# Optimization experiments

Measured on AMD Instinct MI355X. Metric: run time of the kernel, lower is better.

Reference implementation:

```python
import jax, jax.numpy as jnp
import numpy as np

N, B, T, S, E, R = 4, 8, 512, 512, 1024, 1024


def setup_inputs() -> dict:
    key = jax.random.key(0)
    k1, k2, k3, k4, k5 = jax.random.split(key, 5)
    return {
        "query": jax.random.normal(k1, (1, B, T, E), dtype=jnp.float32),
        "key_value_states": jax.random.normal(k2, (N, B, S, R), dtype=jnp.float32),
        "attention_mask": jax.random.normal(k3, (1, B, T, S), dtype=jnp.float32),
        "Wk": jax.random.normal(k4, (E, R), dtype=jnp.float32) * (1.0 / np.sqrt(R)),
        "bk": jax.random.normal(k5, (E,), dtype=jnp.float32) * 0.01,
    }


def reference(query, key_value_states, attention_mask, Wk, bk):
    # k_proj: [N,B,S,R] @ [R,E] + bias -> [N,B,S,E]
    key = jnp.einsum("nbsr,er->nbse", key_value_states, Wk) + bk
    # QK^T (no scaling), query broadcast over N: [N,B,T,S]
    scores = jnp.einsum("bte,nbse->nbts", query[0], key)
    scores = scores + attention_mask  # mask broadcast over N
    attn = jax.nn.softmax(scores, axis=-1)
    # weights @ raw key_value_states (NOT projected key): [N,B,T,R]
    out = jnp.einsum("nbts,nbsr->nbtr", attn, key_value_states)
    return out
```

## Files before the change

### kernel.cpp

```cpp
#include <hip/hip_runtime.h>

typedef unsigned short u16;
typedef unsigned int u32;
typedef unsigned long long u64;

typedef __bf16 bfrag __attribute__((ext_vector_type(8)));
typedef float f32x4 __attribute__((ext_vector_type(4)));

typedef __attribute__((address_space(1))) char* gas1_p;
typedef __attribute__((address_space(3))) char* las3_p;

#define DI __device__ __forceinline__

DI u16 f2bf(float f) {
  u32 u = __float_as_uint(f);
  u += 0x7FFFu + ((u >> 16) & 1u);
  return (u16)(u >> 16);
}
DI float bf2f(u16 h) { return __uint_as_float(((u32)h) << 16); }

DI void gload16(const void* g, void* l) {
  __builtin_amdgcn_global_load_lds((gas1_p)(u64)g, (las3_p)(u32)(u64)l, 16, 0, 0);
}

__global__ __launch_bounds__(256) void k_split4(const float4* __restrict__ in,
                                                uint2* __restrict__ hi,
                                                uint2* __restrict__ lo) {
  int i = blockIdx.x * 256 + threadIdx.x;
  float4 v = in[i];
  u16 h0 = f2bf(v.x), h1 = f2bf(v.y), h2 = f2bf(v.z), h3 = f2bf(v.w);
  u16 l0 = f2bf(v.x - bf2f(h0)), l1 = f2bf(v.y - bf2f(h1));
  u16 l2 = f2bf(v.z - bf2f(h2)), l3 = f2bf(v.w - bf2f(h3));
  hi[i] = make_uint2((u32)h0 | ((u32)h1 << 16), (u32)h2 | ((u32)h3 << 16));
  lo[i] = make_uint2((u32)l0 | ((u32)l1 << 16), (u32)l2 | ((u32)l3 << 16));
}

template <int WH, int WTH, int WTL>
__global__ __launch_bounds__(256) void k_trsplit64(const float* __restrict__ in,
                                                   u16* __restrict__ hi, u16* __restrict__ lo,
                                                   u16* __restrict__ thi, u16* __restrict__ tlo,
                                                   int rows, int cols) {
  __shared__ float tile[64][65];
  const u64 zoff = (u64)blockIdx.z * (u64)rows * (u64)cols;
  const int r0 = threadIdx.x >> 4;
  const int c4 = (threadIdx.x & 15) << 2;
  const float* src = in + zoff + (u64)(blockIdx.y * 64 + r0) * cols + blockIdx.x * 64 + c4;
#pragma unroll
  for (int p = 0; p < 4; ++p) {
    float4 v = *reinterpret_cast<const float4*>(src + (u64)(p * 16) * cols);
    tile[r0 + p * 16][c4 + 0] = v.x;
    tile[r0 + p * 16][c4 + 1] = v.y;
    tile[r0 + p * 16][c4 + 2] = v.z;
    tile[r0 + p * 16][c4 + 3] = v.w;
  }
  __syncthreads();
  if constexpr (WH) {
    const int rr = threadIdx.x >> 3;
    const int cc = (threadIdx.x & 7) << 3;
#pragma unroll
    for (int p = 0; p < 2; ++p) {
      const int r = rr + p * 32;
      u32 h[4], l[4];
#pragma unroll
      for (int j = 0; j < 4; ++j) {
        float a = tile[r][cc + 2 * j], b = tile[r][cc + 2 * j + 1];
        u16 ha = f2bf(a), hb = f2bf(b);
        h[j] = (u32)ha | ((u32)hb << 16);
        l[j] = (u32)f2bf(a - bf2f(ha)) | ((u32)f2bf(b - bf2f(hb)) << 16);
      }
      const u64 o = zoff + (u64)(blockIdx.y * 64 + r) * cols + blockIdx.x * 64 + cc;
      *reinterpret_cast<uint4*>(hi + o) = make_uint4(h[0], h[1], h[2], h[3]);
      *reinterpret_cast<uint4*>(lo + o) = make_uint4(l[0], l[1], l[2], l[3]);
    }
  }
  if constexpr (WTH) {
#pragma unroll
    for (int p = 0; p < 2; ++p) {
      const int id = threadIdx.x + p * 256;
      const int col = id >> 3;
      const int s8 = (id & 7) << 3;
      u32 h[4], l[4];
#pragma unroll
      for (int j = 0; j < 4; ++j) {
        float a = tile[s8 + 2 * j][col], b = tile[s8 + 2 * j + 1][col];
        u16 ha = f2bf(a), hb = f2bf(b);
        h[j] = (u32)ha | ((u32)hb << 16);
        if constexpr (WTL)
          l[j] = (u32)f2bf(a - bf2f(ha)) | ((u32)f2bf(b - bf2f(hb)) << 16);
      }
      const u64 o = zoff + (u64)(blockIdx.x * 64 + col) * rows + blockIdx.y * 64 + s8;
      *reinterpret_cast<uint4*>(thi + o) = make_uint4(h[0], h[1], h[2], h[3]);
      if constexpr (WTL)
        *reinterpret_cast<uint4*>(tlo + o) = make_uint4(l[0], l[1], l[2], l[3]);
    }
  }
}

template <int X3, int FM, int FN, int WR, int WC, int ADDMASK, int SPLITOUT>
__global__ __launch_bounds__(WR * WC * 64, 2) void k_gemm2(
    const u16* __restrict__ Ah, const u16* __restrict__ Al,
    const u16* __restrict__ Bh, const u16* __restrict__ Bl,
    float* __restrict__ Cf, u16* __restrict__ Chi, u16* __restrict__ Clo,
    const float* __restrict__ Mask,
    int K, int N, int mt, int nt,
    u64 aStride, int aMask, u64 bStride, u64 cStride) {
  constexpr int BM = WR * FM * 16, BN = WC * FN * 16;
  constexpr int NTHR = WR * WC * 64;
  constexpr int A_U16 = BM * 32, B_U16 = BN * 32;
  constexpr int AL0 = A_U16;
  constexpr int BH0 = A_U16 * (1 + X3);
  constexpr int TILE = (A_U16 + B_U16) * (1 + X3);
  constexpr int CA = BM * 4 / NTHR;
  constexpr int CB = BN * 4 / NTHR;
  __shared__ u16 lds[2 * TILE];

  const int tid = threadIdx.x, lane = tid & 63;
  const int wid = tid >> 6, wr = wid / WC, wc = wid % WC;

  const int g = (blockIdx.x & 7) * (gridDim.x >> 3) + (blockIdx.x >> 3);
  const int z = g / (mt * nt);
  const int rem = g - z * (mt * nt);
  const int ty = rem / nt, tx = rem - ty * nt;

  const u64 aOff = (u64)(z & aMask) * aStride;
  const u64 bOff = (u64)z * bStride;
  const u16* gA = Ah + aOff + (u64)ty * (u32)BM * (u32)K;
  const u16* gB = Bh + bOff + (u64)tx * (u32)BN * (u32)K;
  const u16* gAl = nullptr;
  const u16* gBl = nullptr;
  if constexpr (X3) {
    gAl = Al + aOff + (u64)ty * (u32)BM * (u32)K;
    gBl = Bl + bOff + (u64)tx * (u32)BN * (u32)K;
  }

  u64 aG[CA];
  u32 aLo[CA];
#pragma unroll
  for (int i = 0; i < CA; ++i) {
    const int c = i * NTHR + tid;
    const int row = c >> 2, ks = c & 3;
    aG[i] = (u64)row * (u32)K + (u32)((ks ^ ((row >> 1) & 3)) << 3);
    aLo[i] = c << 3;
  }
  u64 bG[CB];
  u32 bLo[CB];
#pragma unroll
  for (int i = 0; i < CB; ++i) {
    const int c = i * NTHR + tid;
    const int row = c >> 2, ks = c & 3;
    bG[i] = (u64)row * (u32)K + (u32)((ks ^ ((row >> 1) & 3)) << 3);
    bLo[i] = c << 3;
  }

  f32x4 acc[FM][FN];
#pragma unroll
  for (int m = 0; m < FM; ++m)
#pragma unroll
    for (int n = 0; n < FN; ++n) acc[m][n] = (f32x4){0.f, 0.f, 0.f, 0.f};

  auto STAGE = [&](int bufU, int k0) {
#pragma unroll
    for (int i = 0; i < CA; ++i) {
      gload16(gA + aG[i] + (u32)k0, &lds[bufU + aLo[i]]);
      if constexpr (X3) gload16(gAl + aG[i] + (u32)k0, &lds[bufU + AL0 + aLo[i]]);
    }
#pragma unroll
    for (int i = 0; i < CB; ++i) {
      gload16(gB + bG[i] + (u32)k0, &lds[bufU + BH0 + bLo[i]]);
      if constexpr (X3) gload16(gBl + bG[i] + (u32)k0, &lds[bufU + BH0 + B_U16 + bLo[i]]);
    }
  };

  const int swz = (((lane >> 1) & 3) ^ (lane >> 4)) << 3;
  auto COMPUTE = [&](int bufU) {
    bfrag ah[FM], alr[FM], bh[FN], blr[FN];
#pragma unroll
    for (int m = 0; m < FM; ++m) {
      const int idx = bufU + (wr * (FM * 16) + m * 16 + (lane & 15)) * 32 + swz;
      ah[m] = *reinterpret_cast<const bfrag*>(&lds[idx]);
      if constexpr (X3) alr[m] = *reinterpret_cast<const bfrag*>(&lds[idx + AL0]);
    }
#pragma unroll
    for (int n = 0; n < FN; ++n) {
      const int idx = bufU + BH0 + (wc * (FN * 16) + n * 16 + (lane & 15)) * 32 + swz;
      bh[n] = *reinterpret_cast<const bfrag*>(&lds[idx]);
      if constexpr (X3) blr[n] = *reinterpret_cast<const bfrag*>(&lds[idx + B_U16]);
    }
#pragma unroll
    for (int m = 0; m < FM; ++m)
#pragma unroll
      for (int n = 0; n < FN; ++n) {
        acc[m][n] = __builtin_amdgcn_mfma_f32_16x16x32_bf16(ah[m], bh[n], acc[m][n], 0, 0, 0);
        if constexpr (X3) {
          acc[m][n] = __builtin_amdgcn_mfma_f32_16x16x32_bf16(ah[m], blr[n], acc[m][n], 0, 0, 0);
          acc[m][n] = __builtin_amdgcn_mfma_f32_16x16x32_bf16(alr[m], bh[n], acc[m][n], 0, 0, 0);
        }
      }
  };

  const int NT = K >> 5;
  STAGE(0, 0);
  asm volatile("s_waitcnt vmcnt(0)" ::: "memory");
  __builtin_amdgcn_s_barrier();
  int buf = 0;
  for (int t = 0; t < NT; ++t) {
    if (t + 1 < NT) STAGE(TILE - buf, (t + 1) << 5);
    COMPUTE(buf);
    if (t + 1 < NT) {
      asm volatile("s_waitcnt vmcnt(0)" ::: "memory");
      __builtin_amdgcn_s_barrier();
      buf = TILE - buf;
    }
  }

  const u64 cOff = (u64)z * cStride;
  const u64 mOff = (u64)(z & aMask) * cStride;
  const int rB = ty * BM + wr * (FM * 16) + (lane >> 4) * 4;
  const int cB = tx * BN + wc * (FN * 16) + (lane & 15);
#pragma unroll
  for (int m = 0; m < FM; ++m)
#pragma unroll
    for (int n = 0; n < FN; ++n)
#pragma unroll
      for (int j = 0; j < 4; ++j) {
        const int rr = rB + m * 16 + j, cc = cB + n * 16;
        const u64 ci = cOff + (u64)rr * (u32)N + (u32)cc;
        float v = acc[m][n][j];
        if constexpr (ADDMASK) v += Mask[mOff + (u64)rr * (u32)N + (u32)cc];
        if constexpr (SPLITOUT) {
          u16 h = f2bf(v);
          Chi[ci] = h;
          Clo[ci] = f2bf(v - bf2f(h));
        } else {
          Cf[ci] = v;
        }
      }
}

__global__ __launch_bounds__(256) void k_softmax(const float* __restrict__ sc,
                                                 u16* __restrict__ attn) {
  const int row = blockIdx.x * 4 + (threadIdx.x >> 6);
  const int lane = threadIdx.x & 63;
  const float* srow = sc + (u64)row * 512 + lane * 8;
  float4 s0 = *reinterpret_cast<const float4*>(srow);
  float4 s1 = *reinterpret_cast<const float4*>(srow + 4);
  float x[8] = {s0.x, s0.y, s0.z, s0.w, s1.x, s1.y, s1.z, s1.w};
  float mx = x[0];
#pragma unroll
  for (int j = 1; j < 8; ++j) mx = fmaxf(mx, x[j]);
#pragma unroll
  for (int off = 32; off > 0; off >>= 1) mx = fmaxf(mx, __shfl_xor(mx, off));
  float sum = 0.f;
#pragma unroll
  for (int j = 0; j < 8; ++j) {
    x[j] = __expf(x[j] - mx);
    sum += x[j];
  }
#pragma unroll
  for (int off = 32; off > 0; off >>= 1) sum += __shfl_xor(sum, off);
  const float inv = 1.f / sum;
  u32 o[4];
#pragma unroll
  for (int j = 0; j < 4; ++j) {
    u16 e0 = f2bf(x[2 * j] * inv), e1 = f2bf(x[2 * j + 1] * inv);
    o[j] = (u32)e0 | ((u32)e1 << 16);
  }
  *reinterpret_cast<uint4*>(attn + (u64)row * 512 + lane * 8) = make_uint4(o[0], o[1], o[2], o[3]);
}

extern "C" void kernel_launch(void* const* d_in, const int* in_sizes, int n_in,
                              void* d_out, int out_size, void* d_ws, size_t ws_size,
                              hipStream_t stream) {
  const float* q = (const float*)d_in[0];
  const float* kvs = (const float*)d_in[1];
  const float* mask = (const float*)d_in[2];
  const float* Wk = (const float*)d_in[3];
  float* out = (float*)d_out;

  char* w = (char*)d_ws;
  u16* q_hi = (u16*)(w + 0);
  u16* q_lo = (u16*)(w + 8388608);
  u16* attn = (u16*)(w + 0);
  u16* wkt_hi = (u16*)(w + 16777216);
  u16* wkt_lo = (u16*)(w + 18874368);
  u16* qp_hi = (u16*)(w + 20971520);
  u16* qp_lo = (u16*)(w + 29360128);
  u16* kv_hi = (u16*)(w + 37748736);
  u16* kv_lo = (u16*)(w + 71303168);
  u16* kvt_hi = (u16*)(w + 104857600);
  float* sc = (float*)(w + 138412032);

  k_split4<<<dim3(4096), dim3(256), 0, stream>>>((const float4*)q, (uint2*)q_hi, (uint2*)q_lo);
  k_trsplit64<0, 1, 1><<<dim3(16, 16, 1), dim3(256), 0, stream>>>(
      Wk, (u16*)nullptr, (u16*)nullptr, wkt_hi, wkt_lo, 1024, 1024);
  k_trsplit64<1, 1, 0><<<dim3(16, 8, 32), dim3(256), 0, stream>>>(
      kvs, kv_hi, kv_lo, kvt_hi, (u16*)nullptr, 512, 1024);
  k_gemm2<1, 4, 4, 2, 2, 0, 1><<<dim3(256), dim3(256), 0, stream>>>(
      q_hi, q_lo, wkt_hi, wkt_lo, (float*)nullptr, qp_hi, qp_lo, (const float*)nullptr,
      1024, 1024, 32, 8, (u64)0, 0, (u64)0, (u64)0);
  k_gemm2<1, 4, 4, 2, 2, 1, 0><<<dim3(512), dim3(256), 0, stream>>>(
      qp_hi, qp_lo, kv_hi, kv_lo, sc, (u16*)nullptr, (u16*)nullptr, mask,
      1024, 512, 4, 4, (u64)524288, 7, (u64)524288, (u64)262144);
  k_softmax<<<dim3(4096), dim3(256), 0, stream>>>(sc, attn);
  k_gemm2<0, 8, 4, 2, 2, 0, 0><<<dim3(512), dim3(256), 0, stream>>>(
      attn, (u16*)nullptr, kvt_hi, (u16*)nullptr, out, (u16*)nullptr, (u16*)nullptr,
      (const float*)nullptr, 512, 1024, 2, 8, (u64)262144, 31, (u64)524288, (u64)524288);

  (void)in_sizes; (void)n_in; (void)out_size; (void)ws_size;
}
```

Before: 174.0 us.

## Add 512-thread 256x128 GEMM with triple-buffered LDS pipeline for attention GEMMs

```diff
diff --git a/kernel.cpp b/kernel.cpp
--- a/kernel.cpp
+++ b/kernel.cpp
@@ -21,6 +21,16 @@
 
 DI void gload16(const void* g, void* l) {
   __builtin_amdgcn_global_load_lds((gas1_p)(u64)g, (las3_p)(u32)(u64)l, 16, 0, 0);
+}
+
+template <int N>
+DI void waitvm() {
+  if constexpr (N >= 12)     asm volatile("s_waitcnt vmcnt(12)" ::: "memory");
+  else if constexpr (N == 8) asm volatile("s_waitcnt vmcnt(8)" ::: "memory");
+  else if constexpr (N == 6) asm volatile("s_waitcnt vmcnt(6)" ::: "memory");
+  else if constexpr (N == 4) asm volatile("s_waitcnt vmcnt(4)" ::: "memory");
+  else if constexpr (N == 3) asm volatile("s_waitcnt vmcnt(3)" ::: "memory");
+  else                       asm volatile("s_waitcnt vmcnt(0)" ::: "memory");
 }
 
 __global__ __launch_bounds__(256) void k_split4(const float4* __restrict__ in,
@@ -133,8 +143,7 @@
     gBl = Bl + bOff + (u64)tx * (u32)BN * (u32)K;
   }
 
-  u64 aG[CA];
-  u32 aLo[CA];
+  u64 aG[CA]; u32 aLo[CA];
 #pragma unroll
   for (int i = 0; i < CA; ++i) {
     const int c = i * NTHR + tid;
@@ -142,8 +151,7 @@
     aG[i] = (u64)row * (u32)K + (u32)((ks ^ ((row >> 1) & 3)) << 3);
     aLo[i] = c << 3;
   }
-  u64 bG[CB];
-  u32 bLo[CB];
+  u64 bG[CB]; u32 bLo[CB];
 #pragma unroll
   for (int i = 0; i < CB; ++i) {
     const int c = i * NTHR + tid;
@@ -237,6 +245,148 @@
       }
 }
 
+template <int X3, int ADDMASK, int SPLITOUT, int MINW>
+__global__ __launch_bounds__(512, MINW) void k_gemm3(
+    const u16* __restrict__ Ah, const u16* __restrict__ Al,
+    const u16* __restrict__ Bh, const u16* __restrict__ Bl,
+    float* __restrict__ Cf, u16* __restrict__ Chi, u16* __restrict__ Clo,
+    const float* __restrict__ Mask,
+    int K, int N, int mt, int nt,
+    u64 aStride, int aMask, u64 bStride, u64 cStride) {
+  constexpr int BM = 256, BN = 128, NTHR = 512;
+  constexpr int FM = 4, FN = 4, WC = 2;
+  constexpr int A_U16 = BM * 32, B_U16 = BN * 32;
+  constexpr int AL0 = A_U16;
+  constexpr int BH0 = A_U16 * (1 + X3);
+  constexpr int TILE = (A_U16 + B_U16) * (1 + X3);
+  constexpr int CA = BM * 4 / NTHR;
+  constexpr int CB = BN * 4 / NTHR;
+  constexpr int L = (CA + CB) * (1 + X3);
+  __shared__ u16 lds[3 * TILE];
+
+  const int tid = threadIdx.x, lane = tid & 63;
+  const int wid = tid >> 6, wr = wid >> 1, wc = wid & 1;
+
+  const int g = (blockIdx.x & 7) * (gridDim.x >> 3) + (blockIdx.x >> 3);
+  const int z = g / (mt * nt);
+  const int rem = g - z * (mt * nt);
+  const int ty = rem / nt, tx = rem - ty * nt;
+
+  const u64 aOff = (u64)(z & aMask) * aStride;
+  const u64 bOff = (u64)z * bStride;
+  const u16* gA = Ah + aOff + (u64)ty * (u32)BM * (u32)K;
+  const u16* gB = Bh + bOff + (u64)tx * (u32)BN * (u32)K;
+  const u16* gAl = nullptr;
+  const u16* gBl = nullptr;
+  if constexpr (X3) {
+    gAl = Al + aOff + (u64)ty * (u32)BM * (u32)K;
+    gBl = Bl + bOff + (u64)tx * (u32)BN * (u32)K;
+  }
+
+  u64 aG[CA]; u32 aLo[CA];
+#pragma unroll
+  for (int i = 0; i < CA; ++i) {
+    const int c = i * NTHR + tid;
+    const int row = c >> 2, ks = c & 3;
+    aG[i] = (u64)row * (u32)K + (u32)((ks ^ ((row >> 1) & 3)) << 3);
+    aLo[i] = c << 3;
+  }
+  u64 bG[CB]; u32 bLo[CB];
+#pragma unroll
+  for (int i = 0; i < CB; ++i) {
+    const int c = i * NTHR + tid;
+    const int row = c >> 2, ks = c & 3;
+    bG[i] = (u64)row * (u32)K + (u32)((ks ^ ((row >> 1) & 3)) << 3);
+    bLo[i] = c << 3;
+  }
+
+  f32x4 acc[FM][FN];
+#pragma unroll
+  for (int m = 0; m < FM; ++m)
+#pragma unroll
+    for (int n = 0; n < FN; ++n) acc[m][n] = (f32x4){0.f, 0.f, 0.f, 0.f};
+
+  auto STAGE = [&](int bufU, int k0) {
+#pragma unroll
+    for (int i = 0; i < CA; ++i) {
+      gload16(gA + aG[i] + (u32)k0, &lds[bufU + aLo[i]]);
+      if constexpr (X3) gload16(gAl + aG[i] + (u32)k0, &lds[bufU + AL0 + aLo[i]]);
+    }
+#pragma unroll
+    for (int i = 0; i < CB; ++i) {
+      gload16(gB + bG[i] + (u32)k0, &lds[bufU + BH0 + bLo[i]]);
+      if constexpr (X3) gload16(gBl + bG[i] + (u32)k0, &lds[bufU + BH0 + B_U16 + bLo[i]]);
+    }
+  };
+
+  const int swz = (((lane >> 1) & 3) ^ (lane >> 4)) << 3;
+  auto COMPUTE = [&](int bufU) {
+    bfrag ah[FM], alr[FM], bh[FN], blr[FN];
+#pragma unroll
+    for (int m = 0; m < FM; ++m) {
+      const int idx = bufU + (wr * 64 + m * 16 + (lane & 15)) * 32 + swz;
+      ah[m] = *reinterpret_cast<const bfrag*>(&lds[idx]);
+      if constexpr (X3) alr[m] = *reinterpret_cast<const bfrag*>(&lds[idx + AL0]);
+    }
+#pragma unroll
+    for (int n = 0; n < FN; ++n) {
+      const int idx = bufU + BH0 + (wc * 64 + n * 16 + (lane & 15)) * 32 + swz;
+      bh[n] = *reinterpret_cast<const bfrag*>(&lds[idx]);
+      if constexpr (X3) blr[n] = *reinterpret_cast<const bfrag*>(&lds[idx + B_U16]);
+    }
+#pragma unroll
+    for (int m = 0; m < FM; ++m)
+#pragma unroll
+      for (int n = 0; n < FN; ++n) {
+        acc[m][n] = __builtin_amdgcn_mfma_f32_16x16x32_bf16(ah[m], bh[n], acc[m][n], 0, 0, 0);
+        if constexpr (X3) {
+          acc[m][n] = __builtin_amdgcn_mfma_f32_16x16x32_bf16(ah[m], blr[n], acc[m][n], 0, 0, 0);
+          acc[m][n] = __builtin_amdgcn_mfma_f32_16x16x32_bf16(alr[m], bh[n], acc[m][n], 0, 0, 0);
+        }
+      }
+  };
+
+  const int NT = K >> 5;
+  STAGE(0, 0);
+  STAGE(TILE, 32);
+  STAGE(2 * TILE, 64);
+  int buf = 0;
+  for (int t = 0; t < NT; ++t) {
+    const int w = NT - 1 - t;
+    if (w >= 2)      waitvm<2 * L>();
+    else if (w == 1) waitvm<L>();
+    else             waitvm<0>();
+    __builtin_amdgcn_s_barrier();
+    COMPUTE(buf);
+    __builtin_amdgcn_s_barrier();
+    if (t + 3 < NT) STAGE(buf, (t + 3) << 5);
+    buf = (buf == 2 * TILE) ? 0 : buf + TILE;
+  }
+
+  const u64 cOff = (u64)z * cStride;
+  const u64 mOff = (u64)(z & aMask) * cStride;
+  const int rB = ty * BM + wr * 64 + (lane >> 4) * 4;
+  const int cB = tx * BN + wc * 64 + (lane & 15);
+#pragma unroll
+  for (int m = 0; m < FM; ++m)
+#pragma unroll
+    for (int n = 0; n < FN; ++n)
+#pragma unroll
+      for (int j = 0; j < 4; ++j) {
+        const int rr = rB + m * 16 + j, cc = cB + n * 16;
+        const u64 ci = cOff + (u64)rr * (u32)N + (u32)cc;
+        float v = acc[m][n][j];
+        if constexpr (ADDMASK) v += Mask[mOff + (u64)rr * (u32)N + (u32)cc];
+        if constexpr (SPLITOUT) {
+          u16 h = f2bf(v);
+          Chi[ci] = h;
+          Clo[ci] = f2bf(v - bf2f(h));
+        } else {
+          Cf[ci] = v;
+        }
+      }
+}
+
 __global__ __launch_bounds__(256) void k_softmax(const float* __restrict__ sc,
                                                  u16* __restrict__ attn) {
   const int row = blockIdx.x * 4 + (threadIdx.x >> 6);
@@ -298,11 +448,11 @@
   k_gemm2<1, 4, 4, 2, 2, 0, 1><<<dim3(256), dim3(256), 0, stream>>>(
       q_hi, q_lo, wkt_hi, wkt_lo, (float*)nullptr, qp_hi, qp_lo, (const float*)nullptr,
       1024, 1024, 32, 8, (u64)0, 0, (u64)0, (u64)0);
-  k_gemm2<1, 4, 4, 2, 2, 1, 0><<<dim3(512), dim3(256), 0, stream>>>(
+  k_gemm3<1, 1, 0, 2><<<dim3(256), dim3(512), 0, stream>>>(
       qp_hi, qp_lo, kv_hi, kv_lo, sc, (u16*)nullptr, (u16*)nullptr, mask,
-      1024, 512, 4, 4, (u64)524288, 7, (u64)524288, (u64)262144);
+      1024, 512, 2, 4, (u64)524288, 7, (u64)524288, (u64)262144);
   k_softmax<<<dim3(4096), dim3(256), 0, stream>>>(sc, attn);
-  k_gemm2<0, 8, 4, 2, 2, 0, 0><<<dim3(512), dim3(256), 0, stream>>>(
+  k_gemm3<0, 0, 0, 4><<<dim3(512), dim3(512), 0, stream>>>(
       attn, (u16*)nullptr, kvt_hi, (u16*)nullptr, out, (u16*)nullptr, (u16*)nullptr,
       (const float*)nullptr, 512, 1024, 2, 8, (u64)262144, 31, (u64)524288, (u64)524288);
 
```

Result: no change. 173.2 us (-0.5%).

## Fuse fp32 hi/lo bf16 split into GEMM tile loading for query and kv

Applied to the files above, without the earlier changes.

```diff
diff --git a/kernel.cpp b/kernel.cpp
--- a/kernel.cpp
+++ b/kernel.cpp
@@ -21,18 +21,6 @@
 
 DI void gload16(const void* g, void* l) {
   __builtin_amdgcn_global_load_lds((gas1_p)(u64)g, (las3_p)(u32)(u64)l, 16, 0, 0);
-}
-
-__global__ __launch_bounds__(256) void k_split4(const float4* __restrict__ in,
-                                                uint2* __restrict__ hi,
-                                                uint2* __restrict__ lo) {
-  int i = blockIdx.x * 256 + threadIdx.x;
-  float4 v = in[i];
-  u16 h0 = f2bf(v.x), h1 = f2bf(v.y), h2 = f2bf(v.z), h3 = f2bf(v.w);
-  u16 l0 = f2bf(v.x - bf2f(h0)), l1 = f2bf(v.y - bf2f(h1));
-  u16 l2 = f2bf(v.z - bf2f(h2)), l3 = f2bf(v.w - bf2f(h3));
-  hi[i] = make_uint2((u32)h0 | ((u32)h1 << 16), (u32)h2 | ((u32)h3 << 16));
-  lo[i] = make_uint2((u32)l0 | ((u32)l1 << 16), (u32)l2 | ((u32)l3 << 16));
 }
 
 template <int WH, int WTH, int WTL>
@@ -96,22 +84,24 @@
   }
 }
 
-template <int X3, int FM, int FN, int WR, int WC, int ADDMASK, int SPLITOUT>
-__global__ __launch_bounds__(WR * WC * 64, 2) void k_gemm2(
-    const u16* __restrict__ Ah, const u16* __restrict__ Al,
-    const u16* __restrict__ Bh, const u16* __restrict__ Bl,
+template <int X3, int AF32, int BF32, int FM, int FN, int WR, int WC,
+          int ADDMASK, int SPLITOUT>
+__global__ __launch_bounds__(WR * WC * 64, 2) void k_gemmF(
+    const void* Ap, const u16* Aploi, const void* Bp, const u16* Bploi,
     float* __restrict__ Cf, u16* __restrict__ Chi, u16* __restrict__ Clo,
     const float* __restrict__ Mask,
     int K, int N, int mt, int nt,
     u64 aStride, int aMask, u64 bStride, u64 cStride) {
+  constexpr int NTHR = WR * WC * 64;
   constexpr int BM = WR * FM * 16, BN = WC * FN * 16;
-  constexpr int NTHR = WR * WC * 64;
-  constexpr int A_U16 = BM * 32, B_U16 = BN * 32;
-  constexpr int AL0 = A_U16;
-  constexpr int BH0 = A_U16 * (1 + X3);
-  constexpr int TILE = (A_U16 + B_U16) * (1 + X3);
-  constexpr int CA = BM * 4 / NTHR;
-  constexpr int CB = BN * 4 / NTHR;
+  constexpr int ACH = AF32 ? ((BM * 9 + NTHR - 1) / NTHR) * NTHR : BM * 4;
+  constexpr int BCH = BF32 ? ((BN * 9 + NTHR - 1) / NTHR) * NTHR : BN * 4;
+  constexpr int A_SZ = AF32 ? ACH * 8 : BM * 32 * (1 + X3);
+  constexpr int B_SZ = BF32 ? BCH * 8 : BN * 32 * (1 + X3);
+  constexpr int AL0 = BM * 32;
+  constexpr int BL0 = BN * 32;
+  constexpr int TILE = A_SZ + B_SZ;
+  constexpr int CA = ACH / NTHR, CB = BCH / NTHR;
   __shared__ u16 lds[2 * TILE];
 
   const int tid = threadIdx.x, lane = tid & 63;
@@ -124,32 +114,52 @@
 
   const u64 aOff = (u64)(z & aMask) * aStride;
   const u64 bOff = (u64)z * bStride;
-  const u16* gA = Ah + aOff + (u64)ty * (u32)BM * (u32)K;
-  const u16* gB = Bh + bOff + (u64)tx * (u32)BN * (u32)K;
+  const float* gAf = nullptr;
+  const u16* gA = nullptr;
   const u16* gAl = nullptr;
+  if constexpr (AF32) {
+    gAf = (const float*)Ap + aOff + (u64)ty * (u32)BM * (u32)K;
+  } else {
+    gA = (const u16*)Ap + aOff + (u64)ty * (u32)BM * (u32)K;
+    if constexpr (X3) gAl = Aploi + aOff + (u64)ty * (u32)BM * (u32)K;
+  }
+  const float* gBf = nullptr;
+  const u16* gB = nullptr;
   const u16* gBl = nullptr;
-  if constexpr (X3) {
-    gAl = Al + aOff + (u64)ty * (u32)BM * (u32)K;
-    gBl = Bl + bOff + (u64)tx * (u32)BN * (u32)K;
-  }
-
-  u64 aG[CA];
-  u32 aLo[CA];
+  if constexpr (BF32) {
+    gBf = (const float*)Bp + bOff + (u64)tx * (u32)BN * (u32)K;
+  } else {
+    gB = (const u16*)Bp + bOff + (u64)tx * (u32)BN * (u32)K;
+    if constexpr (X3) gBl = Bploi + bOff + (u64)tx * (u32)BN * (u32)K;
+  }
+
+  u64 aG[CA]; u32 aLd[CA];
 #pragma unroll
   for (int i = 0; i < CA; ++i) {
     const int c = i * NTHR + tid;
-    const int row = c >> 2, ks = c & 3;
-    aG[i] = (u64)row * (u32)K + (u32)((ks ^ ((row >> 1) & 3)) << 3);
-    aLo[i] = c << 3;
-  }
-  u64 bG[CB];
-  u32 bLo[CB];
+    if constexpr (AF32) {
+      const int row = c / 9, cc = c - row * 9;
+      aG[i] = (row < BM && cc < 8) ? ((u64)row * (u32)K + (u32)(cc * 4)) : 0;
+      aLd[i] = c * 8;
+    } else {
+      const int row = c >> 2, ks = c & 3;
+      aG[i] = (u64)row * (u32)K + (u32)((ks ^ ((row >> 1) & 3)) << 3);
+      aLd[i] = c << 3;
+    }
+  }
+  u64 bG[CB]; u32 bLd[CB];
 #pragma unroll
   for (int i = 0; i < CB; ++i) {
     const int c = i * NTHR + tid;
-    const int row = c >> 2, ks = c & 3;
-    bG[i] = (u64)row * (u32)K + (u32)((ks ^ ((row >> 1) & 3)) << 3);
-    bLo[i] = c << 3;
+    if constexpr (BF32) {
+      const int row = c / 9, cc = c - row * 9;
+      bG[i] = (row < BN && cc < 8) ? ((u64)row * (u32)K + (u32)(cc * 4)) : 0;
+      bLd[i] = c * 8;
+    } else {
+      const int row = c >> 2, ks = c & 3;
+      bG[i] = (u64)row * (u32)K + (u32)((ks ^ ((row >> 1) & 3)) << 3);
+      bLd[i] = c << 3;
+    }
   }
 
   f32x4 acc[FM][FN];
@@ -161,30 +171,66 @@
   auto STAGE = [&](int bufU, int k0) {
 #pragma unroll
     for (int i = 0; i < CA; ++i) {
-      gload16(gA + aG[i] + (u32)k0, &lds[bufU + aLo[i]]);
-      if constexpr (X3) gload16(gAl + aG[i] + (u32)k0, &lds[bufU + AL0 + aLo[i]]);
+      if constexpr (AF32) {
+        gload16(gAf + aG[i] + (u32)k0, &lds[bufU + aLd[i]]);
+      } else {
+        gload16(gA + aG[i] + (u32)k0, &lds[bufU + aLd[i]]);
+        if constexpr (X3) gload16(gAl + aG[i] + (u32)k0, &lds[bufU + AL0 + aLd[i]]);
+      }
     }
 #pragma unroll
     for (int i = 0; i < CB; ++i) {
-      gload16(gB + bG[i] + (u32)k0, &lds[bufU + BH0 + bLo[i]]);
-      if constexpr (X3) gload16(gBl + bG[i] + (u32)k0, &lds[bufU + BH0 + B_U16 + bLo[i]]);
+      if constexpr (BF32) {
+        gload16(gBf + bG[i] + (u32)k0, &lds[bufU + A_SZ + bLd[i]]);
+      } else {
+        gload16(gB + bG[i] + (u32)k0, &lds[bufU + A_SZ + bLd[i]]);
+        if constexpr (X3) gload16(gBl + bG[i] + (u32)k0, &lds[bufU + A_SZ + BL0 + bLd[i]]);
+      }
     }
   };
 
   const int swz = (((lane >> 1) & 3) ^ (lane >> 4)) << 3;
   auto COMPUTE = [&](int bufU) {
-    bfrag ah[FM], alr[FM], bh[FN], blr[FN];
+    bfrag ah[FM], al[FM], bh[FN], bl[FN];
 #pragma unroll
     for (int m = 0; m < FM; ++m) {
-      const int idx = bufU + (wr * (FM * 16) + m * 16 + (lane & 15)) * 32 + swz;
-      ah[m] = *reinterpret_cast<const bfrag*>(&lds[idx]);
-      if constexpr (X3) alr[m] = *reinterpret_cast<const bfrag*>(&lds[idx + AL0]);
+      const int row = wr * (FM * 16) + m * 16 + (lane & 15);
+      if constexpr (AF32) {
+        const u32 base = bufU + (u32)row * 72 + (u32)(lane >> 4) * 16;
+        f32x4 p0 = *reinterpret_cast<const f32x4*>(&lds[base]);
+        f32x4 p1 = *reinterpret_cast<const f32x4*>(&lds[base + 8]);
+#pragma unroll
+        for (int j = 0; j < 8; ++j) {
+          float f = j < 4 ? p0[j] : p1[j - 4];
+          __bf16 h = (__bf16)f;
+          ah[m][j] = h;
+          al[m][j] = (__bf16)(f - (float)h);
+        }
+      } else {
+        const int idx = bufU + row * 32 + swz;
+        ah[m] = *reinterpret_cast<const bfrag*>(&lds[idx]);
+        if constexpr (X3) al[m] = *reinterpret_cast<const bfrag*>(&lds[idx + AL0]);
+      }
     }
 #pragma unroll
     for (int n = 0; n < FN; ++n) {
-      const int idx = bufU + BH0 + (wc * (FN * 16) + n * 16 + (lane & 15)) * 32 + swz;
-      bh[n] = *reinterpret_cast<const bfrag*>(&lds[idx]);
-      if constexpr (X3) blr[n] = *reinterpret_cast<const bfrag*>(&lds[idx + B_U16]);
+      const int row = wc * (FN * 16) + n * 16 + (lane & 15);
+      if constexpr (BF32) {
+        const u32 base = bufU + A_SZ + (u32)row * 72 + (u32)(lane >> 4) * 16;
+        f32x4 p0 = *reinterpret_cast<const f32x4*>(&lds[base]);
+        f32x4 p1 = *reinterpret_cast<const f32x4*>(&lds[base + 8]);
+#pragma unroll
+        for (int j = 0; j < 8; ++j) {
+          float f = j < 4 ? p0[j] : p1[j - 4];
+          __bf16 h = (__bf16)f;
+          bh[n][j] = h;
+          bl[n][j] = (__bf16)(f - (float)h);
+        }
+      } else {
+        const int idx = bufU + A_SZ + row * 32 + swz;
+        bh[n] = *reinterpret_cast<const bfrag*>(&lds[idx]);
+        if constexpr (X3) bl[n] = *reinterpret_cast<const bfrag*>(&lds[idx + BL0]);
+      }
     }
 #pragma unroll
     for (int m = 0; m < FM; ++m)
@@ -192,8 +238,8 @@
       for (int n = 0; n < FN; ++n) {
         acc[m][n] = __builtin_amdgcn_mfma_f32_16x16x32_bf16(ah[m], bh[n], acc[m][n], 0, 0, 0);
         if constexpr (X3) {
-          acc[m][n] = __builtin_amdgcn_mfma_f32_16x16x32_bf16(ah[m], blr[n], acc[m][n], 0, 0, 0);
-          acc[m][n] = __builtin_amdgcn_mfma_f32_16x16x32_bf16(alr[m], bh[n], acc[m][n], 0, 0, 0);
+          acc[m][n] = __builtin_amdgcn_mfma_f32_16x16x32_bf16(ah[m], bl[n], acc[m][n], 0, 0, 0);
+          acc[m][n] = __builtin_amdgcn_mfma_f32_16x16x32_bf16(al[m], bh[n], acc[m][n], 0, 0, 0);
         }
       }
   };
@@ -278,33 +324,31 @@
   float* out = (float*)d_out;
 
   char* w = (char*)d_ws;
-  u16* q_hi = (u16*)(w + 0);
-  u16* q_lo = (u16*)(w + 8388608);
   u16* attn = (u16*)(w + 0);
   u16* wkt_hi = (u16*)(w + 16777216);
   u16* wkt_lo = (u16*)(w + 18874368);
   u16* qp_hi = (u16*)(w + 20971520);
   u16* qp_lo = (u16*)(w + 29360128);
-  u16* kv_hi = (u16*)(w + 37748736);
-  u16* kv_lo = (u16*)(w + 71303168);
   u16* kvt_hi = (u16*)(w + 104857600);
   float* sc = (float*)(w + 138412032);
 
-  k_split4<<<dim3(4096), dim3(256), 0, stream>>>((const float4*)q, (uint2*)q_hi, (uint2*)q_lo);
   k_trsplit64<0, 1, 1><<<dim3(16, 16, 1), dim3(256), 0, stream>>>(
       Wk, (u16*)nullptr, (u16*)nullptr, wkt_hi, wkt_lo, 1024, 1024);
-  k_trsplit64<1, 1, 0><<<dim3(16, 8, 32), dim3(256), 0, stream>>>(
-      kvs, kv_hi, kv_lo, kvt_hi, (u16*)nullptr, 512, 1024);
-  k_gemm2<1, 4, 4, 2, 2, 0, 1><<<dim3(256), dim3(256), 0, stream>>>(
-      q_hi, q_lo, wkt_hi, wkt_lo, (float*)nullptr, qp_hi, qp_lo, (const float*)nullptr,
+  k_trsplit64<0, 1, 0><<<dim3(16, 8, 32), dim3(256), 0, stream>>>(
+      kvs, (u16*)nullptr, (u16*)nullptr, kvt_hi, (u16*)nullptr, 512, 1024);
+  k_gemmF<1, 1, 0, 4, 4, 2, 2, 0, 1><<<dim3(256), dim3(256), 0, stream>>>(
+      q, (const u16*)nullptr, wkt_hi, wkt_lo,
+      (float*)nullptr, qp_hi, qp_lo, (const float*)nullptr,
       1024, 1024, 32, 8, (u64)0, 0, (u64)0, (u64)0);
-  k_gemm2<1, 4, 4, 2, 2, 1, 0><<<dim3(512), dim3(256), 0, stream>>>(
-      qp_hi, qp_lo, kv_hi, kv_lo, sc, (u16*)nullptr, (u16*)nullptr, mask,
+  k_gemmF<1, 0, 1, 4, 4, 2, 2, 1, 0><<<dim3(512), dim3(256), 0, stream>>>(
+      qp_hi, qp_lo, kvs, (const u16*)nullptr,
+      sc, (u16*)nullptr, (u16*)nullptr, mask,
       1024, 512, 4, 4, (u64)524288, 7, (u64)524288, (u64)262144);
   k_softmax<<<dim3(4096), dim3(256), 0, stream>>>(sc, attn);
-  k_gemm2<0, 8, 4, 2, 2, 0, 0><<<dim3(512), dim3(256), 0, stream>>>(
-      attn, (u16*)nullptr, kvt_hi, (u16*)nullptr, out, (u16*)nullptr, (u16*)nullptr,
-      (const float*)nullptr, 512, 1024, 2, 8, (u64)262144, 31, (u64)524288, (u64)524288);
+  k_gemmF<0, 0, 0, 8, 4, 2, 2, 0, 0><<<dim3(512), dim3(256), 0, stream>>>(
+      attn, (const u16*)nullptr, kvt_hi, (const u16*)nullptr,
+      out, (u16*)nullptr, (u16*)nullptr, (const float*)nullptr,
+      512, 1024, 2, 8, (u64)262144, 31, (u64)524288, (u64)524288);
 
   (void)in_sizes; (void)n_in; (void)out_size; (void)ws_size;
 }
```

New measurement: 159.5 us, median of 2. 8.3% less time.
